# Performance work log

Measured on AMD Instinct MI355X. Metric: run time of the kernel, lower is better.

Reference implementation:

```python
import jax, jax.numpy as jnp
import numpy as np

D_MODEL = 1024
N_HEADS = 16
D_HEAD = D_MODEL // N_HEADS
B, S = 2, 2048


def setup_inputs() -> dict:
    key = jax.random.key(0)
    ks = jax.random.split(key, 8)
    scale = 1.0 / np.sqrt(D_MODEL)
    return {
        "x": jax.random.normal(ks[0], (B, S, D_MODEL), dtype=jnp.float32),
        "Wq": jax.random.normal(ks[1], (D_MODEL, D_MODEL), dtype=jnp.float32) * scale,
        "bq": jnp.zeros((D_MODEL,), dtype=jnp.float32),
        "Wk": jax.random.normal(ks[2], (D_MODEL, D_MODEL), dtype=jnp.float32) * scale,
        "bk": jnp.zeros((D_MODEL,), dtype=jnp.float32),
        "Wv": jax.random.normal(ks[3], (D_MODEL, D_MODEL), dtype=jnp.float32) * scale,
        "bv": jnp.zeros((D_MODEL,), dtype=jnp.float32),
        "Wo": jax.random.normal(ks[4], (D_MODEL, D_MODEL), dtype=jnp.float32) * scale,
    }


def reference(x, Wq, bq, Wk, bk, Wv, bv, Wo):
    Bsz, Slen, D = x.shape
    # projections -> [B, H, S, Dh]
    def split_heads(t):
        return t.reshape(Bsz, Slen, N_HEADS, D_HEAD).transpose(0, 2, 1, 3)
    q = split_heads(x @ Wq + bq)
    k = split_heads(x @ Wk + bk)
    v = split_heads(x @ Wv + bv)
    scale = jnp.sqrt(jnp.float32(D_HEAD))
    scores = jnp.einsum('bhsd,bhtd->bhst', q, k) / scale  # [B,H,S,S]
    causal_mask = jnp.tril(jnp.ones((Slen, Slen), dtype=jnp.bool_))
    scores = jnp.where(causal_mask, scores, jnp.finfo(scores.dtype).min)
    attn = jax.nn.softmax(scores, axis=-1)
    # deterministic=True path: dropout is identity
    out = jnp.einsum('bhst,bhtd->bhsd', attn, v)
    out = out.transpose(0, 2, 1, 3).reshape(Bsz, Slen, D)
    return out @ Wo
```

## Files before the change

kernel.cpp:

```cpp
#include <hip/hip_runtime.h>
#include <hip/hip_bf16.h>

#define BATCH   2
#define SEQ     2048
#define DMODEL  1024
#define NHEADS  16
#define DHEAD   64
#define MROWS   (BATCH*SEQ)
#define NBH     (BATCH*NHEADS)

typedef float  f32x4  __attribute__((ext_vector_type(4)));
typedef short  s16x4  __attribute__((ext_vector_type(4)));
typedef short  s16x8  __attribute__((ext_vector_type(8)));
typedef __bf16 bf16x8 __attribute__((ext_vector_type(8)));

__device__ __forceinline__ short f2bf(float f) {
  union { float f; unsigned u; } v; v.f = f;
  return (short)((v.u + 0x7fffu + ((v.u >> 16) & 1u)) >> 16);
}
__device__ __forceinline__ float bf2f(short s) {
  union { unsigned u; float f; } v; v.u = ((unsigned)(unsigned short)s) << 16;
  return v.f;
}

__global__ void prep_fused(const float* __restrict__ x, short* __restrict__ xb,
                           const float* __restrict__ Wq, const float* __restrict__ Wk,
                           const float* __restrict__ Wv, const float* __restrict__ Wo,
                           short* __restrict__ WtQKV, short* __restrict__ WtO) {
  __shared__ float t[32][33];
  int z = blockIdx.z;
  int tx = threadIdx.x, ty = threadIdx.y;
  if (z >= 4) {
    int blk = (z - 4) * 1024 + blockIdx.y * 32 + blockIdx.x;
    int i = (blk * 256 + ty * 32 + tx) * 4;
    float4 v = *(const float4*)(x + i);
    s16x4 o = { f2bf(v.x), f2bf(v.y), f2bf(v.z), f2bf(v.w) };
    *(s16x4*)(xb + i) = o;
    return;
  }
  const float* W; short* Wt;
  if      (z == 0) { W = Wq; Wt = WtQKV; }
  else if (z == 1) { W = Wk; Wt = WtQKV + (1u << 20); }
  else if (z == 2) { W = Wv; Wt = WtQKV + (2u << 20); }
  else             { W = Wo; Wt = WtO; }
  int n0 = blockIdx.x * 32, k0 = blockIdx.y * 32;
  #pragma unroll
  for (int i = 0; i < 32; i += 8) t[ty + i][tx] = W[(k0 + ty + i) * DMODEL + n0 + tx];
  __syncthreads();
  #pragma unroll
  for (int i = 0; i < 32; i += 8) Wt[(n0 + ty + i) * DMODEL + k0 + tx] = f2bf(t[tx][ty + i]);
}

template<int MT, int NT, int EPI>
__global__ __launch_bounds__(256) void gemm_bf16(
    const short* __restrict__ A, const short* __restrict__ Bt,
    const float* __restrict__ bq, const float* __restrict__ bk, const float* __restrict__ bv,
    short* __restrict__ qb, short* __restrict__ kb, short* __restrict__ vt,
    float* __restrict__ out)
{
  constexpr int K = DMODEL, BK = 32;
  constexpr int WM = MT / 2, WN = NT / 2;
  constexpr int TM = WM / 16, TN = WN / 16;
  constexpr int CA = MT * BK / 512;
  constexpr int CB = NT * BK / 512;
  constexpr int TP = 136;
  constexpr int SME = (EPI == 0) ? 128 * TP : (MT * BK + NT * BK);
  __shared__ short smem[SME];
  short* la = smem;
  short* lb = smem + MT * BK;
  const int tid = threadIdx.x;
  const int wave = tid >> 6, lane = tid & 63;
  const int quad = lane >> 4, l16 = lane & 15;
  const int wr = wave >> 1, wc = wave & 1;
  const int nx = gridDim.x, ny = gridDim.y;
  const int g = blockIdx.y * nx + blockIdx.x;
  const int xcd = g & 7, rr = g >> 3;
  const int m0 = (xcd * (ny >> 3) + rr / nx) * MT;
  const int n0 = (rr % nx) * NT;
  const int arow = lane >> 2, acol = (lane & 3) * 8;

  f32x4 acc[TM][TN] = {};

  for (int k0 = 0; k0 < K; k0 += BK) {
    for (int c = wave; c < CA; c += 4) {
      const short* gp = A + (m0 + c * 16 + arow) * K + k0 + acol;
      __builtin_amdgcn_global_load_lds((__attribute__((address_space(1))) void*)gp,
                                       (__attribute__((address_space(3))) void*)(la + c * 512),
                                       16, 0, 0);
    }
    for (int c = wave; c < CB; c += 4) {
      const short* gp = Bt + (n0 + c * 16 + arow) * K + k0 + acol;
      __builtin_amdgcn_global_load_lds((__attribute__((address_space(1))) void*)gp,
                                       (__attribute__((address_space(3))) void*)(lb + c * 512),
                                       16, 0, 0);
    }
    __syncthreads();
    bf16x8 af[TM], bfr[TN];
    #pragma unroll
    for (int i = 0; i < TM; ++i)
      af[i] = *(const bf16x8*)&la[(wr * WM + i * 16 + l16) * BK + quad * 8];
    #pragma unroll
    for (int j = 0; j < TN; ++j)
      bfr[j] = *(const bf16x8*)&lb[(wc * WN + j * 16 + l16) * BK + quad * 8];
    #pragma unroll
    for (int i = 0; i < TM; ++i)
      #pragma unroll
      for (int j = 0; j < TN; ++j)
        acc[i][j] = __builtin_amdgcn_mfma_f32_16x16x32_bf16(af[i], bfr[j], acc[i][j], 0, 0, 0);
    __syncthreads();
  }

  if constexpr (EPI == 0) {
    const bool isV = (n0 >= 2 * DMODEL);
    const float* bias; int nbase; float scl;
    if (n0 < DMODEL)          { bias = bq; nbase = 0;          scl = 0.125f * 1.44269504089f; }
    else if (n0 < 2 * DMODEL) { bias = bk; nbase = DMODEL;     scl = 1.f; }
    else                      { bias = bv; nbase = 2 * DMODEL; scl = 1.f; }
    #pragma unroll
    for (int j = 0; j < TN; ++j) {
      int coll = wc * WN + j * 16 + l16;
      float bias_v = bias[n0 - nbase + coll];
      #pragma unroll
      for (int i = 0; i < TM; ++i) {
        int rowl = wr * WM + i * 16 + quad * 4;
        #pragma unroll
        for (int r = 0; r < 4; ++r) {
          short v = f2bf((acc[i][j][r] + bias_v) * scl);
          if (isV) smem[coll * TP + rowl + r] = v;
          else     smem[(rowl + r) * TP + coll] = v;
        }
      }
    }
    __syncthreads();
    const int b = m0 >> 11, s0 = m0 & (SEQ - 1);
    const int rseg = tid & 15, rrow = tid >> 4;
    if (!isV) {
      short* dst = (n0 < DMODEL) ? qb : kb;
      #pragma unroll
      for (int it = 0; it < 8; ++it) {
        int row = it * 16 + rrow;
        int colg = (n0 - nbase) + rseg * 8;
        int h = colg >> 6, d = colg & 63;
        s16x8 v = *(const s16x8*)&smem[row * TP + rseg * 8];
        *(s16x8*)(dst + ((b * NHEADS + h) * SEQ + s0 + row) * DHEAD + d) = v;
      }
    } else {
      #pragma unroll
      for (int it = 0; it < 8; ++it) {
        int drow = it * 16 + rrow;
        int colg = (n0 - nbase) + drow;
        int h = colg >> 6, d = colg & 63;
        s16x8 v = *(const s16x8*)&smem[drow * TP + rseg * 8];
        *(s16x8*)(vt + ((b * NHEADS + h) * DHEAD + d) * SEQ + s0 + rseg * 8) = v;
      }
    }
  } else {
    #pragma unroll
    for (int i = 0; i < TM; ++i)
      #pragma unroll
      for (int r = 0; r < 4; ++r) {
        int mrow = m0 + wr * WM + i * 16 + quad * 4 + r;
        #pragma unroll
        for (int j = 0; j < TN; ++j)
          out[mrow * DMODEL + n0 + wc * WN + j * 16 + l16] = acc[i][j][r];
      }
    (void)bq; (void)bk; (void)bv; (void)qb; (void)kb; (void)vt;
  }
}


__global__ __launch_bounds__(256, 2) void attn_k(
    const short* __restrict__ qbp, const short* __restrict__ kbp,
    const short* __restrict__ vtb, short* __restrict__ oP, float* __restrict__ lP)
{
  __shared__ short kls[2][8192];
  __shared__ short vls[2][8192];
  const int tid = threadIdx.x, wave = tid >> 6, lane = tid & 63;
  const int quad = lane >> 4, l16 = lane & 15;
  const int half = blockIdx.x & 1;
  const int bh = (blockIdx.x >> 1) & 31;
  const int qg = blockIdx.x >> 6;
  const int qt1 = qg * 8 + wave * 2;
  const int mF[4] = { qt1 * 16, (qt1 + 1) * 16, (126 - qt1) * 16, (127 - qt1) * 16 };
  const int nch = (127 - 8 * qg) / 4 + 1;
  const short* Q  = qbp + bh * SEQ * DHEAD;
  const short* Kp = kbp + bh * SEQ * DHEAD;
  const short* Vt = vtb + bh * DHEAD * SEQ;

  bf16x8 qf[4][2];
  #pragma unroll
  for (int f = 0; f < 4; ++f) {
    qf[f][0] = *(const bf16x8*)&Q[(mF[f] + l16) * DHEAD + quad * 8];
    qf[f][1] = *(const bf16x8*)&Q[(mF[f] + l16) * DHEAD + 32 + quad * 8];
  }

  float lF[4] = {};
  f32x4 oF[4][4] = {};

  const int vdl = lane >> 3, vsl = lane & 7;

  auto stage1 = [&](int buf, int slot, int t0) {
    #pragma unroll
    for (int j = 0; j < 2; ++j) {
      int g = j * 4 + wave;
      const short* gp = Kp + (t0 + lane) * DHEAD + g * 8;
      __builtin_amdgcn_global_load_lds((__attribute__((address_space(1))) void*)gp,
                                       (__attribute__((address_space(3))) void*)&kls[buf][slot * 4096 + g * 512],
                                       16, 0, 0);
    }
    #pragma unroll
    for (int j = 0; j < 2; ++j) {
      int gd = j * 4 + wave;
      const short* gp = Vt + (gd * 8 + vdl) * SEQ + t0 + ((vsl ^ vdl) * 8);
      __builtin_amdgcn_global_load_lds((__attribute__((address_space(1))) void*)gp,
                                       (__attribute__((address_space(3))) void*)&vls[buf][slot * 4096 + gd * 512],
                                       16, 0, 0);
    }
  };
  auto stagepair = [&](int buf, int cc) {
    stage1(buf, 0, cc * 64);
    if (cc + 2 < nch) stage1(buf, 1, (cc + 2) * 64);
  };

  stagepair(0, half);
  int it = 0;
  for (int cc = half; cc < nch; cc += 4, ++it) {
    __syncthreads();
    if (cc + 4 < nch) stagepair((it + 1) & 1, cc + 4);
    const int buf = it & 1;
    #pragma unroll
    for (int u = 0; u < 2; ++u) {
      const int c = cc + 2 * u;
      if (c < nch) {
        const int t0 = c * 64;
        const int sb = u * 4096;
        #pragma unroll
        for (int t = 0; t < 4; ++t) {
          const int tb = t0 + t * 16;
          if (tb <= mF[3]) {
            bf16x8 kf0 = *(const bf16x8*)&kls[buf][sb + ((0 + quad) * 64 + t * 16 + l16) * 8];
            bf16x8 kf1 = *(const bf16x8*)&kls[buf][sb + ((4 + quad) * 64 + t * 16 + l16) * 8];
            s16x4 vf[4];
            {
              int gsw = ((t * 2 + (quad >> 1)) ^ (l16 & 7));
              #pragma unroll
              for (int dt = 0; dt < 4; ++dt)
                vf[dt] = *(const s16x4*)&vls[buf][sb + ((dt * 16 + l16) * 8 + gsw) * 8 + (quad & 1) * 4];
            }
            #pragma unroll
            for (int f = 0; f < 4; ++f) {
              if (tb <= mF[f]) {
                f32x4 a = {};
                a = __builtin_amdgcn_mfma_f32_16x16x32_bf16(kf0, qf[f][0], a, 0, 0, 0);
                a = __builtin_amdgcn_mfma_f32_16x16x32_bf16(kf1, qf[f][1], a, 0, 0, 0);
                if (tb == mF[f]) {
                  #pragma unroll
                  for (int r = 0; r < 4; ++r)
                    if (quad * 4 + r > l16) a[r] = -1e30f;
                }
                f32x4 p;
                #pragma unroll
                for (int r = 0; r < 4; ++r) p[r] = __builtin_amdgcn_exp2f(a[r]);
                lF[f] += (p[0] + p[1]) + (p[2] + p[3]);
                __hip_bfloat162 c01 = __float22bfloat162_rn(float2{p[0], p[1]});
                __hip_bfloat162 c23 = __float22bfloat162_rn(float2{p[2], p[3]});
                union { unsigned u2[2]; s16x4 s; } pu;
                pu.u2[0] = *(unsigned*)&c01; pu.u2[1] = *(unsigned*)&c23;
                #pragma unroll
                for (int dt = 0; dt < 4; ++dt)
                  oF[f][dt] = __builtin_amdgcn_mfma_f32_16x16x16bf16_1k(pu.s, vf[dt], oF[f][dt], 0, 0, 0);
              }
            }
          }
        }
      }
    }
  }

  float* lD = lP + (half * NBH + bh) * SEQ;
  short* oD = oP + ((half * NBH + bh) * SEQ) * DHEAD;
  #pragma unroll
  for (int f = 0; f < 4; ++f) {
    float l = lF[f];
    l += __shfl_xor(l, 16, 64); l += __shfl_xor(l, 32, 64);
    if (quad == 0) lD[mF[f] + l16] = l;
    #pragma unroll
    for (int r = 0; r < 4; ++r) {
      int s = mF[f] + quad * 4 + r;
      #pragma unroll
      for (int dt = 0; dt < 4; ++dt)
        oD[s * DHEAD + dt * 16 + l16] = f2bf(oF[f][dt][r]);
    }
  }
}

__global__ void attn_merge(const short* __restrict__ oP, const float* __restrict__ lP,
                           short* __restrict__ ob) {
  int idx = blockIdx.x * 256 + threadIdx.x;
  int d8 = idx & 7, s = (idx >> 3) & (SEQ - 1), bh = idx >> 14;
  s16x8 e = *(const s16x8*)&oP[((0   + bh) * SEQ + s) * DHEAD + d8 * 8];
  s16x8 o = *(const s16x8*)&oP[((NBH + bh) * SEQ + s) * DHEAD + d8 * 8];
  float linv = 1.0f / (lP[bh * SEQ + s] + lP[(NBH + bh) * SEQ + s]);
  s16x8 r;
  #pragma unroll
  for (int k = 0; k < 8; ++k) r[k] = f2bf((bf2f(e[k]) + bf2f(o[k])) * linv);
  int b = bh >> 4, h = bh & 15;
  *(s16x8*)&ob[(b * SEQ + s) * DMODEL + h * DHEAD + d8 * 8] = r;
}

extern "C" void kernel_launch(void* const* d_in, const int* in_sizes, int n_in,
                              void* d_out, int out_size, void* d_ws, size_t ws_size,
                              hipStream_t stream) {
  const float* x  = (const float*)d_in[0];
  const float* Wq = (const float*)d_in[1];
  const float* bq = (const float*)d_in[2];
  const float* Wk = (const float*)d_in[3];
  const float* bk = (const float*)d_in[4];
  const float* Wv = (const float*)d_in[5];
  const float* bv = (const float*)d_in[6];
  const float* Wo = (const float*)d_in[7];
  float* out = (float*)d_out;

  char* ws = (char*)d_ws;
  short* xb  = (short*)(ws);
  short* wtq = (short*)(ws + (8u  << 20));
  short* wto = (short*)(ws + (14u << 20));
  short* qb  = (short*)(ws + (16u << 20));
  short* kb  = (short*)(ws + (24u << 20));
  short* vt  = (short*)(ws + (32u << 20));
  short* ob  = (short*)(ws + (40u << 20));
  short* oP  = (short*)(ws + (48u << 20));
  float* lP  = (float*)(ws + (80u << 20));

  prep_fused<<<dim3(32, 32, 8), dim3(32, 8), 0, stream>>>(x, xb, Wq, Wk, Wv, Wo, wtq, wto);

  gemm_bf16<128, 128, 0><<<dim3(3 * DMODEL / 128, MROWS / 128), 256, 0, stream>>>(
      xb, wtq, bq, bk, bv, qb, kb, vt, nullptr);

  attn_k<<<8 * NBH * 2, 256, 0, stream>>>(qb, kb, vt, oP, lP);
  attn_merge<<<NBH * SEQ * 8 / 256, 256, 0, stream>>>(oP, lP, ob);

  gemm_bf16<64, 128, 1><<<dim3(DMODEL / 128, MROWS / 64), 256, 0, stream>>>(
      ob, wto, nullptr, nullptr, nullptr, nullptr, nullptr, nullptr, out);
}
```

Before: 188.0 us.

## Fuse split-KV merge into attention kernel via atomic last-arriver flags

Removes the separate attn_merge kernel. Each attention block atomically increments a per-(q-group, head) flag, and the second block to finish combines its own partial output with the other half's partial from global memory, writing the final bf16 output. The block-to-work mapping is also reordered so the two halves of a pair are scheduled with mirrored q-group order, which spreads out load. In exchange it adds a memset launch, thread fences and an atomic per block, while still writing and reading the partial buffers.

```diff
diff --git a/kernel.cpp b/kernel.cpp
--- a/kernel.cpp
+++ b/kernel.cpp
@@ -171,15 +171,17 @@
 
 __global__ __launch_bounds__(256, 2) void attn_k(
     const short* __restrict__ qbp, const short* __restrict__ kbp,
-    const short* __restrict__ vtb, short* __restrict__ oP, float* __restrict__ lP)
+    const short* __restrict__ vtb, short* __restrict__ oP, float* __restrict__ lP,
+    short* __restrict__ ob, int* __restrict__ flags)
 {
   __shared__ short kls[2][8192];
   __shared__ short vls[2][8192];
   const int tid = threadIdx.x, wave = tid >> 6, lane = tid & 63;
   const int quad = lane >> 4, l16 = lane & 15;
-  const int half = blockIdx.x & 1;
-  const int bh = (blockIdx.x >> 1) & 31;
-  const int qg = blockIdx.x >> 6;
+  const int half = blockIdx.x >> 8;
+  const int r8 = blockIdx.x & 255;
+  const int qg = half ? 7 - (r8 >> 5) : (r8 >> 5);
+  const int bh = r8 & 31;
   const int qt1 = qg * 8 + wave * 2;
   const int mF[4] = { qt1 * 16, (qt1 + 1) * 16, (126 - qt1) * 16, (127 - qt1) * 16 };
   const int nch = (127 - 8 * qg) / 4 + 1;
@@ -283,6 +285,7 @@
   for (int f = 0; f < 4; ++f) {
     float l = lF[f];
     l += __shfl_xor(l, 16, 64); l += __shfl_xor(l, 32, 64);
+    lF[f] = l;
     if (quad == 0) lD[mF[f] + l16] = l;
     #pragma unroll
     for (int r = 0; r < 4; ++r) {
@@ -292,20 +295,33 @@
         oD[s * DHEAD + dt * 16 + l16] = f2bf(oF[f][dt][r]);
     }
   }
-}
-
-__global__ void attn_merge(const short* __restrict__ oP, const float* __restrict__ lP,
-                           short* __restrict__ ob) {
-  int idx = blockIdx.x * 256 + threadIdx.x;
-  int d8 = idx & 7, s = (idx >> 3) & (SEQ - 1), bh = idx >> 14;
-  s16x8 e = *(const s16x8*)&oP[((0   + bh) * SEQ + s) * DHEAD + d8 * 8];
-  s16x8 o = *(const s16x8*)&oP[((NBH + bh) * SEQ + s) * DHEAD + d8 * 8];
-  float linv = 1.0f / (lP[bh * SEQ + s] + lP[(NBH + bh) * SEQ + s]);
-  s16x8 r;
-  #pragma unroll
-  for (int k = 0; k < 8; ++k) r[k] = f2bf((bf2f(e[k]) + bf2f(o[k])) * linv);
-  int b = bh >> 4, h = bh & 15;
-  *(s16x8*)&ob[(b * SEQ + s) * DMODEL + h * DHEAD + d8 * 8] = r;
+
+  __threadfence();
+  __syncthreads();
+  __shared__ int win;
+  if (tid == 0) win = (atomicAdd(&flags[qg * 32 + bh], 1) == 1);
+  __syncthreads();
+  if (!win) return;
+  __threadfence();
+  const int oh = 1 - half;
+  const short* oO = oP + ((oh * NBH + bh) * SEQ) * DHEAD;
+  const float* lO = lP + (oh * NBH + bh) * SEQ;
+  const int b = bh >> 4, h = bh & 15;
+  #pragma unroll
+  for (int f = 0; f < 4; ++f) {
+    #pragma unroll
+    for (int r = 0; r < 4; ++r) {
+      int s = mF[f] + quad * 4 + r;
+      float lown = __shfl(lF[f], quad * 4 + r, 64);
+      float linv = 1.0f / (lown + lO[s]);
+      #pragma unroll
+      for (int dt = 0; dt < 4; ++dt) {
+        float other = bf2f(oO[s * DHEAD + dt * 16 + l16]);
+        ob[(b * SEQ + s) * DMODEL + h * DHEAD + dt * 16 + l16] =
+            f2bf((oF[f][dt][r] + other) * linv);
+      }
+    }
+  }
 }
 
 extern "C" void kernel_launch(void* const* d_in, const int* in_sizes, int n_in,
@@ -331,14 +347,16 @@
   short* ob  = (short*)(ws + (40u << 20));
   short* oP  = (short*)(ws + (48u << 20));
   float* lP  = (float*)(ws + (80u << 20));
+  int*   flg = (int*)  (ws + (81u << 20));
+
+  hipMemsetAsync(flg, 0, 256 * sizeof(int), stream);
 
   prep_fused<<<dim3(32, 32, 8), dim3(32, 8), 0, stream>>>(x, xb, Wq, Wk, Wv, Wo, wtq, wto);
 
   gemm_bf16<128, 128, 0><<<dim3(3 * DMODEL / 128, MROWS / 128), 256, 0, stream>>>(
       xb, wtq, bq, bk, bv, qb, kb, vt, nullptr);
 
-  attn_k<<<8 * NBH * 2, 256, 0, stream>>>(qb, kb, vt, oP, lP);
-  attn_merge<<<NBH * SEQ * 8 / 256, 256, 0, stream>>>(oP, lP, ob);
+  attn_k<<<8 * NBH * 2, 256, 0, stream>>>(qb, kb, vt, oP, lP, ob, flg);
 
   gemm_bf16<64, 128, 1><<<dim3(DMODEL / 128, MROWS / 64), 256, 0, stream>>>(
       ob, wto, nullptr, nullptr, nullptr, nullptr, nullptr, nullptr, out);
```

Result: slower. 286.4 us (+52.3%).
